# Kernel optimization log

Hardware: AMD Instinct MI355X
Metric: run time of the kernel (lower is better)

## Reference

```python
import jax, jax.numpy as jnp
import numpy as np

POOL_LIST = (1, 2, 4)  # pyramid levels -> 1x1, 2x2, 4x4 bins


def _spp_mix(x, pool_list=POOL_LIST):
    """Spatial pyramid pooling, pool_type='mix' (max + mean), channels_last.

    x: (B, H, W, C) -> (B, sum(p*p for p in pool_list) * C)
    Matches the original TF loop ordering: for each level, outer loop over
    bin columns (jy), inner loop over bin rows (ix).
    """
    B, H, W, C = x.shape
    outs = []
    for p in pool_list:
        wr, wc = H // p, W // p  # window rows/cols (floor div, as in original)
        # crop to covered region, then split into p x p bins in one reshape
        xs = x[:, :p * wr, :p * wc, :].reshape(B, p, wr, p, wc, C)
        # mix = max + mean over each window
        v = xs.max(axis=(2, 4)) + xs.mean(axis=(2, 4))  # (B, pr, pc, C)
        # original appends in (jy outer, ix inner) order -> transpose rows/cols
        v = jnp.transpose(v, (0, 2, 1, 3)).reshape(B, p * p * C)
        outs.append(v)
    return jnp.concatenate(outs, axis=-1)


def setup_inputs() -> dict:
    key = jax.random.key(0)
    x = jax.random.normal(key, (32, 64, 64, 512), dtype=jnp.float32)
    return {"x": x}


def reference(x) -> jnp.ndarray:
    return _spp_mix(x)
```

## Files before the change

### kernel.cpp

```cpp
#include <hip/hip_runtime.h>
#include <math.h>


#define B_ 32
#define HW_ 64
#define C_ 512
#define CVEC 128

__device__ __forceinline__ float4 f4max(float4 a, float4 b) {
    return make_float4(fmaxf(a.x, b.x), fmaxf(a.y, b.y),
                       fmaxf(a.z, b.z), fmaxf(a.w, b.w));
}
__device__ __forceinline__ float4 f4add(float4 a, float4 b) {
    return make_float4(a.x + b.x, a.y + b.y, a.z + b.z, a.w + b.w);
}
__device__ __forceinline__ float4 f4mix(float4 m, float4 s, float inv) {
    return make_float4(m.x + s.x * inv, m.y + s.y * inv,
                       m.z + s.z * inv, m.w + s.w * inv);
}

__global__ __launch_bounds__(256) void spp_rows_kernel(
    const float4* __restrict__ x,
    float4* __restrict__ rmax,
    float4* __restrict__ rsum)
{
    const int blk = blockIdx.x;
    const int t   = threadIdx.x;
    const float4* row = x + (size_t)blk * (HW_ * CVEC);

    float4 m[4], s[4];
    #pragma unroll
    for (int bc = 0; bc < 4; ++bc) {
        m[bc] = make_float4(-INFINITY, -INFINITY, -INFINITY, -INFINITY);
        s[bc] = make_float4(0.f, 0.f, 0.f, 0.f);
        #pragma unroll
        for (int k8 = 0; k8 < 8; ++k8) {
            const float4 v = row[(bc * 8 + k8) * 256 + t];
            m[bc] = f4max(m[bc], v);
            s[bc] = f4add(s[bc], v);
        }
    }

    __shared__ float4 lm[4][CVEC];
    __shared__ float4 ls[4][CVEC];
    if (t >= CVEC) {
        #pragma unroll
        for (int bc = 0; bc < 4; ++bc) { lm[bc][t - CVEC] = m[bc]; ls[bc][t - CVEC] = s[bc]; }
    }
    __syncthreads();
    if (t < CVEC) {
        #pragma unroll
        for (int bc = 0; bc < 4; ++bc) {
            m[bc] = f4max(m[bc], lm[bc][t]);
            s[bc] = f4add(s[bc], ls[bc][t]);
            const int o = (blk * 4 + bc) * CVEC + t;
            rmax[o] = m[bc];
            rsum[o] = s[bc];
        }
    }
}

__global__ __launch_bounds__(256) void spp_bins_kernel(
    const float4* __restrict__ rmax,
    const float4* __restrict__ rsum,
    float4* __restrict__ bmax,
    float4* __restrict__ bsum,
    float4* __restrict__ out)
{
    const int blk = blockIdx.x;
    const int b   = blk >> 4;
    const int bin = blk & 15;
    const int br  = bin >> 2;
    const int bc  = bin & 3;
    const int t   = threadIdx.x;
    const int cg  = t & (CVEC - 1);
    const int ih  = t >> 7;

    float4 m = make_float4(-INFINITY, -INFINITY, -INFINITY, -INFINITY);
    float4 s = make_float4(0.f, 0.f, 0.f, 0.f);
    #pragma unroll
    for (int r = 0; r < 8; ++r) {
        const int i = br * 16 + ih * 8 + r;
        const int o = ((b * HW_ + i) * 4 + bc) * CVEC + cg;
        m = f4max(m, rmax[o]);
        s = f4add(s, rsum[o]);
    }

    __shared__ float4 lm[CVEC];
    __shared__ float4 ls[CVEC];
    if (ih) { lm[cg] = m; ls[cg] = s; }
    __syncthreads();
    if (!ih) {
        m = f4max(m, lm[cg]);
        s = f4add(s, ls[cg]);
        const int o = (b * 16 + bin) * CVEC + cg;
        bmax[o] = m;
        bsum[o] = s;
        out[b * (21 * CVEC) + 5 * CVEC + (bc * 4 + br) * CVEC + cg] =
            f4mix(m, s, 1.0f / 256.0f);
    }
}

__global__ __launch_bounds__(256) void spp_agg_kernel(
    const float4* __restrict__ bmax,
    const float4* __restrict__ bsum,
    float4* __restrict__ out)
{
    const int idx = blockIdx.x * 256 + threadIdx.x;
    const int b   = idx >> 7;
    const int cg  = idx & (CVEC - 1);
    const int pbase = b * 16 * CVEC + cg;
    const int row   = b * (21 * CVEC);

    float4 m1 = make_float4(-INFINITY, -INFINITY, -INFINITY, -INFINITY);
    float4 s1 = make_float4(0.f, 0.f, 0.f, 0.f);
    #pragma unroll
    for (int pr = 0; pr < 2; ++pr) {
        #pragma unroll
        for (int pc = 0; pc < 2; ++pc) {
            float4 mm = make_float4(-INFINITY, -INFINITY, -INFINITY, -INFINITY);
            float4 ss = make_float4(0.f, 0.f, 0.f, 0.f);
            #pragma unroll
            for (int dr = 0; dr < 2; ++dr) {
                #pragma unroll
                for (int dc = 0; dc < 2; ++dc) {
                    const int bb = (2 * pr + dr) * 4 + (2 * pc + dc);
                    mm = f4max(mm, bmax[pbase + bb * CVEC]);
                    ss = f4add(ss, bsum[pbase + bb * CVEC]);
                }
            }
            out[row + CVEC + (pc * 2 + pr) * CVEC + cg] =
                f4mix(mm, ss, 1.0f / 1024.0f);
            m1 = f4max(m1, mm);
            s1 = f4add(s1, ss);
        }
    }
    out[row + cg] = f4mix(m1, s1, 1.0f / 4096.0f);
}

extern "C" void kernel_launch(void* const* d_in, const int* in_sizes, int n_in,
                              void* d_out, int out_size, void* d_ws, size_t ws_size,
                              hipStream_t stream) {
    const float4* x = (const float4*)d_in[0];
    float* ws = (float*)d_ws;
    float4* rmax = (float4*)ws;
    float4* rsum = (float4*)(ws + (size_t)B_ * HW_ * 4 * C_);
    float4* bmax = (float4*)(ws + (size_t)2 * B_ * HW_ * 4 * C_);
    float4* bsum = (float4*)(ws + (size_t)2 * B_ * HW_ * 4 * C_ + B_ * 16 * C_);
    float4* out = (float4*)d_out;

    spp_rows_kernel<<<B_ * HW_, 256, 0, stream>>>(x, rmax, rsum);
    spp_bins_kernel<<<B_ * 16, 256, 0, stream>>>(rmax, rsum, bmax, bsum, out);
    spp_agg_kernel<<<(B_ * CVEC) / 256, 256, 0, stream>>>(bmax, bsum, out);
}
```

Baseline: 369.5 us.

## Reduce row pairs in first pass and fuse bin and aggregate kernels

```diff
diff --git a/kernel.cpp b/kernel.cpp
--- a/kernel.cpp
+++ b/kernel.cpp
@@ -19,14 +19,14 @@
                        m.z + s.z * inv, m.w + s.w * inv);
 }
 
-__global__ __launch_bounds__(256) void spp_rows_kernel(
+__global__ __launch_bounds__(256) void spp_pairs_kernel(
     const float4* __restrict__ x,
-    float4* __restrict__ rmax,
-    float4* __restrict__ rsum)
+    float4* __restrict__ pmax,
+    float4* __restrict__ psum)
 {
     const int blk = blockIdx.x;
     const int t   = threadIdx.x;
-    const float4* row = x + (size_t)blk * (HW_ * CVEC);
+    const float4* slab = x + (size_t)blk * (2 * HW_ * CVEC);
 
     float4 m[4], s[4];
     #pragma unroll
@@ -35,9 +35,11 @@
         s[bc] = make_float4(0.f, 0.f, 0.f, 0.f);
         #pragma unroll
         for (int k8 = 0; k8 < 8; ++k8) {
-            const float4 v = row[(bc * 8 + k8) * 256 + t];
-            m[bc] = f4max(m[bc], v);
-            s[bc] = f4add(s[bc], v);
+            const int o = (bc * 8 + k8) * 256 + t;
+            const float4 v0 = slab[o];
+            const float4 v1 = slab[o + HW_ * CVEC];
+            m[bc] = f4max(m[bc], f4max(v0, v1));
+            s[bc] = f4add(s[bc], f4add(v0, v1));
         }
     }
 
@@ -54,88 +56,70 @@
             m[bc] = f4max(m[bc], lm[bc][t]);
             s[bc] = f4add(s[bc], ls[bc][t]);
             const int o = (blk * 4 + bc) * CVEC + t;
-            rmax[o] = m[bc];
-            rsum[o] = s[bc];
+            pmax[o] = m[bc];
+            psum[o] = s[bc];
         }
     }
 }
 
-__global__ __launch_bounds__(256) void spp_bins_kernel(
-    const float4* __restrict__ rmax,
-    const float4* __restrict__ rsum,
-    float4* __restrict__ bmax,
-    float4* __restrict__ bsum,
+__global__ __launch_bounds__(512) void spp_agg_kernel(
+    const float4* __restrict__ pmax,
+    const float4* __restrict__ psum,
     float4* __restrict__ out)
 {
-    const int blk = blockIdx.x;
-    const int b   = blk >> 4;
-    const int bin = blk & 15;
-    const int br  = bin >> 2;
-    const int bc  = bin & 3;
-    const int t   = threadIdx.x;
-    const int cg  = t & (CVEC - 1);
-    const int ih  = t >> 7;
+    const int b  = blockIdx.x;
+    const int t  = threadIdx.x;
+    const int br = t >> 7;
+    const int cg = t & (CVEC - 1);
+    const int row = b * (21 * CVEC);
 
-    float4 m = make_float4(-INFINITY, -INFINITY, -INFINITY, -INFINITY);
-    float4 s = make_float4(0.f, 0.f, 0.f, 0.f);
+    __shared__ float4 lm[16][CVEC];
+    __shared__ float4 ls[16][CVEC];
+
     #pragma unroll
-    for (int r = 0; r < 8; ++r) {
-        const int i = br * 16 + ih * 8 + r;
-        const int o = ((b * HW_ + i) * 4 + bc) * CVEC + cg;
-        m = f4max(m, rmax[o]);
-        s = f4add(s, rsum[o]);
-    }
-
-    __shared__ float4 lm[CVEC];
-    __shared__ float4 ls[CVEC];
-    if (ih) { lm[cg] = m; ls[cg] = s; }
-    __syncthreads();
-    if (!ih) {
-        m = f4max(m, lm[cg]);
-        s = f4add(s, ls[cg]);
-        const int o = (b * 16 + bin) * CVEC + cg;
-        bmax[o] = m;
-        bsum[o] = s;
-        out[b * (21 * CVEC) + 5 * CVEC + (bc * 4 + br) * CVEC + cg] =
+    for (int bc = 0; bc < 4; ++bc) {
+        float4 m = make_float4(-INFINITY, -INFINITY, -INFINITY, -INFINITY);
+        float4 s = make_float4(0.f, 0.f, 0.f, 0.f);
+        #pragma unroll
+        for (int p8 = 0; p8 < 8; ++p8) {
+            const int pair = br * 8 + p8;
+            const int o = ((b * 32 + pair) * 4 + bc) * CVEC + cg;
+            m = f4max(m, pmax[o]);
+            s = f4add(s, psum[o]);
+        }
+        lm[br * 4 + bc][cg] = m;
+        ls[br * 4 + bc][cg] = s;
+        out[row + 5 * CVEC + (bc * 4 + br) * CVEC + cg] =
             f4mix(m, s, 1.0f / 256.0f);
     }
-}
+    __syncthreads();
 
-__global__ __launch_bounds__(256) void spp_agg_kernel(
-    const float4* __restrict__ bmax,
-    const float4* __restrict__ bsum,
-    float4* __restrict__ out)
-{
-    const int idx = blockIdx.x * 256 + threadIdx.x;
-    const int b   = idx >> 7;
-    const int cg  = idx & (CVEC - 1);
-    const int pbase = b * 16 * CVEC + cg;
-    const int row   = b * (21 * CVEC);
-
-    float4 m1 = make_float4(-INFINITY, -INFINITY, -INFINITY, -INFINITY);
-    float4 s1 = make_float4(0.f, 0.f, 0.f, 0.f);
-    #pragma unroll
-    for (int pr = 0; pr < 2; ++pr) {
+    if (t < CVEC) {
+        float4 m1 = make_float4(-INFINITY, -INFINITY, -INFINITY, -INFINITY);
+        float4 s1 = make_float4(0.f, 0.f, 0.f, 0.f);
         #pragma unroll
-        for (int pc = 0; pc < 2; ++pc) {
-            float4 mm = make_float4(-INFINITY, -INFINITY, -INFINITY, -INFINITY);
-            float4 ss = make_float4(0.f, 0.f, 0.f, 0.f);
+        for (int pr = 0; pr < 2; ++pr) {
             #pragma unroll
-            for (int dr = 0; dr < 2; ++dr) {
+            for (int pc = 0; pc < 2; ++pc) {
+                float4 mm = make_float4(-INFINITY, -INFINITY, -INFINITY, -INFINITY);
+                float4 ss = make_float4(0.f, 0.f, 0.f, 0.f);
                 #pragma unroll
-                for (int dc = 0; dc < 2; ++dc) {
-                    const int bb = (2 * pr + dr) * 4 + (2 * pc + dc);
-                    mm = f4max(mm, bmax[pbase + bb * CVEC]);
-                    ss = f4add(ss, bsum[pbase + bb * CVEC]);
+                for (int dr = 0; dr < 2; ++dr) {
+                    #pragma unroll
+                    for (int dc = 0; dc < 2; ++dc) {
+                        const int bin = (2 * pr + dr) * 4 + (2 * pc + dc);
+                        mm = f4max(mm, lm[bin][cg]);
+                        ss = f4add(ss, ls[bin][cg]);
+                    }
                 }
+                out[row + CVEC + (pc * 2 + pr) * CVEC + cg] =
+                    f4mix(mm, ss, 1.0f / 1024.0f);
+                m1 = f4max(m1, mm);
+                s1 = f4add(s1, ss);
             }
-            out[row + CVEC + (pc * 2 + pr) * CVEC + cg] =
-                f4mix(mm, ss, 1.0f / 1024.0f);
-            m1 = f4max(m1, mm);
-            s1 = f4add(s1, ss);
         }
+        out[row + cg] = f4mix(m1, s1, 1.0f / 4096.0f);
     }
-    out[row + cg] = f4mix(m1, s1, 1.0f / 4096.0f);
 }
 
 extern "C" void kernel_launch(void* const* d_in, const int* in_sizes, int n_in,
@@ -143,13 +127,10 @@
                               hipStream_t stream) {
     const float4* x = (const float4*)d_in[0];
     float* ws = (float*)d_ws;
-    float4* rmax = (float4*)ws;
-    float4* rsum = (float4*)(ws + (size_t)B_ * HW_ * 4 * C_);
-    float4* bmax = (float4*)(ws + (size_t)2 * B_ * HW_ * 4 * C_);
-    float4* bsum = (float4*)(ws + (size_t)2 * B_ * HW_ * 4 * C_ + B_ * 16 * C_);
+    float4* pmax = (float4*)ws;
+    float4* psum = (float4*)(ws + (size_t)B_ * 32 * 4 * C_);
     float4* out = (float4*)d_out;
 
-    spp_rows_kernel<<<B_ * HW_, 256, 0, stream>>>(x, rmax, rsum);
-    spp_bins_kernel<<<B_ * 16, 256, 0, stream>>>(rmax, rsum, bmax, bsum, out);
-    spp_agg_kernel<<<(B_ * CVEC) / 256, 256, 0, stream>>>(bmax, bsum, out);
+    spp_pairs_kernel<<<B_ * 32, 256, 0, stream>>>(x, pmax, psum);
+    spp_agg_kernel<<<B_, 512, 0, stream>>>(pmax, psum, out);
 }
```

Measured after the change: 361.7 us. 1.02x faster.
